# Kernel optimization log

Hardware: AMD Instinct MI355X
Metric: run time of the kernel (lower is better)

The kernel has to match this reference:

```python
import jax, jax.numpy as jnp
import numpy as np

B, S, E, H = 2, 2048, 1024, 16
D = E // H  # head_dim = 64

def setup_inputs() -> dict:
    key = jax.random.key(0)
    k1, k2, k3 = jax.random.split(key, 3)
    x = jax.random.normal(k1, (B, S, E), dtype=jnp.float32)
    W_attn = jax.random.normal(k2, (E, 3 * E), dtype=jnp.float32) * 0.02
    b_attn = jnp.zeros((3 * E,), dtype=jnp.float32)
    W_proj = jax.random.normal(k3, (E, E), dtype=jnp.float32) * 0.02
    b_proj = jnp.zeros((E,), dtype=jnp.float32)
    return {"x": x, "W_attn": W_attn, "b_attn": b_attn, "W_proj": W_proj, "b_proj": b_proj}

def reference(x, W_attn, b_attn, W_proj, b_proj):
    bsz, seq, emb = x.shape
    # fused QKV projection (Conv1D == linear with [in,out] weight)
    qkv = x @ W_attn + b_attn                       # [B,S,3E]
    q, k, v = jnp.split(qkv, 3, axis=-1)
    def to_heads(t):
        return t.reshape(bsz, seq, H, D).transpose(0, 2, 1, 3)  # [B,H,S,D]
    q, k, v = to_heads(q), to_heads(k), to_heads(v)
    scale = jnp.float32(D) ** -0.5
    scores = jnp.einsum('bhqd,bhkd->bhqk', q, k) * scale        # [B,H,S,S]
    causal = jnp.tril(jnp.ones((seq, seq), dtype=bool))
    scores = jnp.where(causal, scores, jnp.float32(-jnp.inf))
    attn = jax.nn.softmax(scores, axis=-1)
    out = jnp.einsum('bhqk,bhkd->bhqd', attn, v)                # [B,H,S,D]
    out = out.transpose(0, 2, 1, 3).reshape(bsz, seq, emb)
    y = out @ W_proj + b_proj
    return y
```

## Files before the change

kernel.cpp:

```cpp
#include <hip/hip_runtime.h>
#include <hip/hip_bf16.h>


typedef __bf16 bf16;
typedef __bf16 bf16x4 __attribute__((ext_vector_type(4)));
typedef __bf16 bf16x8 __attribute__((ext_vector_type(8)));
typedef float  f32x4  __attribute__((ext_vector_type(4)));

#define MNEG (-1.0e30f)
#define QSCALE 0.1803368801f

__device__ __forceinline__ void gload16(const bf16* g, bf16* l) {
  __builtin_amdgcn_global_load_lds((const __attribute__((address_space(1))) void*)g,
                                   (__attribute__((address_space(3))) void*)l, 16, 0, 0);
}

__global__ __launch_bounds__(256) void prep_k(const float* __restrict__ x, bf16* __restrict__ xb,
                                              const float* __restrict__ Wa, bf16* __restrict__ WaT,
                                              const float* __restrict__ Wp, bf16* __restrict__ WpT) {
  const int bid = blockIdx.x;
  if (bid < 2048) {
    const int i = bid * 256 + threadIdx.x;
    f32x4 a = ((const f32x4*)x)[2 * i], b = ((const f32x4*)x)[2 * i + 1];
    bf16x8 o;
    for (int j = 0; j < 4; ++j) { o[j] = (bf16)a[j]; o[4 + j] = (bf16)b[j]; }
    ((bf16x8*)xb)[i] = o;
    return;
  }
  __shared__ bf16 t[64][68];
  const float* in; bf16* out; int C, cx, cy;
  if (bid < 2816) { in = Wa; out = WaT; C = 3072; const int tt = bid - 2048; cx = tt % 48; cy = tt / 48; }
  else            { in = Wp; out = WpT; C = 1024; const int tt = bid - 2816; cx = tt % 16; cy = tt / 16; }
  const int R = 1024;
  const int c0 = cx * 64, r0 = cy * 64;
  const int lr = threadIdx.x >> 4;
  const int lc = (threadIdx.x & 15) * 4;
  for (int i = 0; i < 4; ++i) {
    int r = lr + i * 16;
    f32x4 v = *(const f32x4*)(in + (size_t)(r0 + r) * C + c0 + lc);
    bf16x4 b;
    for (int j = 0; j < 4; ++j) b[j] = (bf16)v[j];
    *(bf16x4*)&t[r][lc] = b;
  }
  __syncthreads();
  for (int i = 0; i < 4; ++i) {
    int c = lr + i * 16;
    bf16x4 v;
    for (int j = 0; j < 4; ++j) v[j] = t[lc + j][c];
    *(bf16x4*)(out + (size_t)(c0 + c) * R + r0 + lc) = v;
  }
}

__global__ __launch_bounds__(512) void gemm_qkv(const bf16* __restrict__ A,
                                                const bf16* __restrict__ Bt,
                                                const float* __restrict__ bias,
                                                bf16* __restrict__ Qo,
                                                bf16* __restrict__ Ko,
                                                bf16* __restrict__ Vo,
                                                int M, int N, int K) {
  __shared__ bf16 As[2][128 * 32];
  __shared__ bf16 Bs[2][128 * 32];
  const int tid = threadIdx.x;
  const int w = tid >> 6, l = tid & 63;
  const int nx = gridDim.x;
  const int nwg = nx * gridDim.y;
  const int flat = blockIdx.y * nx + blockIdx.x;
  const int swz = (flat & 7) * (nwg >> 3) + (flat >> 3);
  const int m0 = (swz / nx) * 128, n0 = (swz % nx) * 128;
  const int wm = w >> 2, wn = w & 3;
  const int fr = l & 15, fg = l >> 4;
  const int grow = tid >> 2;
  const int gcol = (tid & 3) * 8;

  f32x4 acc[4][2] = {};

  auto stage = [&](int k0, int buf) {
    gload16(A  + (size_t)(m0 + grow) * K + k0 + gcol, As[buf] + 512 * w);
    gload16(Bt + (size_t)(n0 + grow) * K + k0 + gcol, Bs[buf] + 512 * w);
  };

  stage(0, 0);

  int cur = 0;
  for (int k0 = 0; k0 < K; k0 += 32) {
    const bool havenext = (k0 + 32 < K);
    if (havenext) stage(k0 + 32, cur ^ 1);

    if (havenext) asm volatile("s_waitcnt vmcnt(2)" ::: "memory");
    else          asm volatile("s_waitcnt vmcnt(0)" ::: "memory");
    __builtin_amdgcn_s_barrier();
    asm volatile("" ::: "memory");

    const bf16* as = As[cur];
    const bf16* bs = Bs[cur];
    bf16x8 af[4], bfv[2];
    for (int mt = 0; mt < 4; ++mt)
      af[mt] = *(const bf16x8*)(as + (wm * 64 + mt * 16 + fr) * 32 + 8 * fg);
    for (int nt = 0; nt < 2; ++nt)
      bfv[nt] = *(const bf16x8*)(bs + (wn * 32 + nt * 16 + fr) * 32 + 8 * fg);
    for (int mt = 0; mt < 4; ++mt)
      for (int nt = 0; nt < 2; ++nt)
        acc[mt][nt] = __builtin_amdgcn_mfma_f32_16x16x32_bf16(af[mt], bfv[nt], acc[mt][nt], 0, 0, 0);

    asm volatile("s_waitcnt lgkmcnt(0)" ::: "memory");
    __builtin_amdgcn_sched_barrier(0);
    __builtin_amdgcn_s_barrier();
    cur ^= 1;
  }

  for (int mt = 0; mt < 4; ++mt) {
    for (int nt = 0; nt < 2; ++nt) {
      const int row0 = m0 + wm * 64 + mt * 16 + 4 * fg;
      const int col = n0 + wn * 32 + nt * 16 + fr;
      const float bv = bias[col];
      const int which = col >> 10, h = (col >> 6) & 15, d = col & 63;
      const int b = row0 >> 11, s = row0 & 2047;
      if (which == 2) {
        bf16x4 vv;
        for (int r = 0; r < 4; ++r) vv[r] = (bf16)(acc[mt][nt][r] + bv);
        *(bf16x4*)(Vo + ((size_t)(b * 16 + h) * 64 + d) * 2048 + s) = vv;
      } else if (which == 0) {
        for (int r = 0; r < 4; ++r)
          Qo[((size_t)(b * 16 + h) * 2048 + s + r) * 64 + d] =
              (bf16)((acc[mt][nt][r] + bv) * QSCALE);
      } else {
        for (int r = 0; r < 4; ++r)
          Ko[((size_t)(b * 16 + h) * 2048 + s + r) * 64 + d] = (bf16)(acc[mt][nt][r] + bv);
      }
    }
  }
}

__global__ __launch_bounds__(512) void gemm_proj(const bf16* __restrict__ A,
                                                 const bf16* __restrict__ Bt,
                                                 const float* __restrict__ bias,
                                                 float* __restrict__ C,
                                                 int M, int N, int K) {
  constexpr int BN = 64, WN = 2, WM = 4, MR = 32, MT = 2;
  __shared__ bf16 As0[128 * 32], As1[128 * 32];
  __shared__ bf16 Bs0[BN * 32],  Bs1[BN * 32];
  const int tid = threadIdx.x;
  const int w = tid >> 6, l = tid & 63;
  const int nx = gridDim.x;
  const int nwg = nx * gridDim.y;
  const int flat = blockIdx.y * nx + blockIdx.x;
  const int swz = (flat & 7) * (nwg >> 3) + (flat >> 3);
  const int m0 = (swz / nx) * 128, n0 = (swz % nx) * BN;
  const int wm = w / WN, wn = w % WN;
  const int fr = l & 15, fg = l >> 4;
  const int grow = tid >> 2;
  const int gcol = (tid & 3) * 8;

  f32x4 acc[MT][2] = {};

  for (int k0 = 0; k0 < K; k0 += 64) {
    __syncthreads();
    gload16(A + (size_t)(m0 + grow) * K + k0 + gcol,      As0 + 512 * w);
    gload16(A + (size_t)(m0 + grow) * K + k0 + 32 + gcol, As1 + 512 * w);
    if (w < 4) {
      gload16(Bt + (size_t)(n0 + grow) * K + k0 + gcol,      Bs0 + 512 * w);
      gload16(Bt + (size_t)(n0 + grow) * K + k0 + 32 + gcol, Bs1 + 512 * w);
    }
    __syncthreads();

    bf16x8 af[MT][2], bfv[2][2];
    for (int mt = 0; mt < MT; ++mt) {
      af[mt][0] = *(const bf16x8*)(As0 + (wm * MR + mt * 16 + fr) * 32 + 8 * fg);
      af[mt][1] = *(const bf16x8*)(As1 + (wm * MR + mt * 16 + fr) * 32 + 8 * fg);
    }
    for (int nt = 0; nt < 2; ++nt) {
      bfv[nt][0] = *(const bf16x8*)(Bs0 + (wn * 32 + nt * 16 + fr) * 32 + 8 * fg);
      bfv[nt][1] = *(const bf16x8*)(Bs1 + (wn * 32 + nt * 16 + fr) * 32 + 8 * fg);
    }
    for (int mt = 0; mt < MT; ++mt)
      for (int nt = 0; nt < 2; ++nt) {
        acc[mt][nt] = __builtin_amdgcn_mfma_f32_16x16x32_bf16(af[mt][0], bfv[nt][0], acc[mt][nt], 0, 0, 0);
        acc[mt][nt] = __builtin_amdgcn_mfma_f32_16x16x32_bf16(af[mt][1], bfv[nt][1], acc[mt][nt], 0, 0, 0);
      }
  }

  for (int mt = 0; mt < MT; ++mt)
    for (int nt = 0; nt < 2; ++nt) {
      const int row0 = m0 + wm * MR + mt * 16 + 4 * fg;
      const int col = n0 + wn * 32 + nt * 16 + fr;
      const float bv = bias[col];
      for (int r = 0; r < 4; ++r)
        C[(size_t)(row0 + r) * N + col] = acc[mt][nt][r] + bv;
    }
}

__global__ __launch_bounds__(256, 3) void attn_k(const bf16* __restrict__ Qw,
                                                 const bf16* __restrict__ Kw,
                                                 const bf16* __restrict__ VtG,
                                                 bf16* __restrict__ AO) {
  __shared__ bf16 Ks[128 * 72];
  __shared__ bf16 Vt[64 * 136];
  __shared__ bf16 Ps[4 * 16 * 72];
  const int tid = threadIdx.x, w = tid >> 6, l = tid & 63;
  const int bid = blockIdx.x;
  const int bh = ((bid & 7) << 2) | ((bid >> 3) & 3);
  const int qt = 31 - (bid >> 5);
  const int q0 = qt * 64;
  const int fr = l & 15, fg = l >> 4;
  const size_t base = (size_t)bh * 2048 * 64;
  const int qw0 = q0 + w * 16;
  const int q = qw0 + fr;
  bf16* Pw = Ps + w * 16 * 72;
  const int r8 = tid >> 3, c8 = (tid & 7) * 8;
  const int r16 = tid >> 4, c16 = (tid & 15) * 8;

  bf16x8 qf[2];
  for (int t = 0; t < 2; ++t)
    qf[t] = *(const bf16x8*)(Qw + base + (size_t)(qw0 + fr) * 64 + 32 * t + 8 * fg);

  f32x4 oacc[4] = {};
  float lsum = 0.f;
  bf16x8 kreg[4], vreg[4];

  auto load_tile = [&](int kt) {
    for (int c = 0; c < 4; ++c) {
      kreg[c] = *(const bf16x8*)(Kw + base + (size_t)(kt + r8 + 32 * c) * 64 + c8);
      vreg[c] = *(const bf16x8*)(VtG + base + (size_t)(r16 + 16 * c) * 2048 + kt + c16);
    }
  };
  auto write_tile = [&]() {
    for (int c = 0; c < 4; ++c) {
      *(bf16x8*)(Ks + (r8 + 32 * c) * 72 + c8) = kreg[c];
      *(bf16x8*)(Vt + (r16 + 16 * c) * 136 + c16) = vreg[c];
    }
  };

  load_tile(0);
  write_tile();
  __syncthreads();

  for (int kt = 0; kt <= q0; kt += 128) {
    const bool havenext = (kt + 128 <= q0);
    if (havenext) load_tile(kt + 128);

    for (int h = 0; h < 2; ++h) {
      const int kh = kt + 64 * h;
      if (kh > q0) break;

      f32x4 sc[4];
      __builtin_amdgcn_s_setprio(1);
      for (int c = 0; c < 4; ++c) {
        bf16x8 kf0 = *(const bf16x8*)(Ks + (64 * h + c * 16 + fr) * 72 + 8 * fg);
        bf16x8 kf1 = *(const bf16x8*)(Ks + (64 * h + c * 16 + fr) * 72 + 32 + 8 * fg);
        f32x4 z = {};
        z = __builtin_amdgcn_mfma_f32_16x16x32_bf16(kf0, qf[0], z, 0, 0, 0);
        sc[c] = __builtin_amdgcn_mfma_f32_16x16x32_bf16(kf1, qf[1], z, 0, 0, 0);
      }
      __builtin_amdgcn_s_setprio(0);

      const bool need_mask = (kh + 63 > qw0);
      float psum = 0.f;
      for (int c = 0; c < 4; ++c) {
        bf16x4 pb;
        for (int r = 0; r < 4; ++r) {
          float s = sc[c][r];
          if (need_mask && (kh + c * 16 + 4 * fg + r > q)) s = MNEG;
          const float pv = __builtin_amdgcn_exp2f(s);
          psum += pv;
          pb[r] = (bf16)pv;
        }
        *(bf16x4*)(Pw + fr * 72 + c * 16 + 4 * fg) = pb;
      }
      psum += __shfl_xor(psum, 16, 64);
      psum += __shfl_xor(psum, 32, 64);
      lsum += psum;

      asm volatile("" ::: "memory");
      __builtin_amdgcn_s_setprio(1);
      for (int t = 0; t < 2; ++t) {
        bf16x8 pa = *(const bf16x8*)(Pw + fr * 72 + 32 * t + 8 * fg);
        for (int dt = 0; dt < 4; ++dt) {
          bf16x8 vf = *(const bf16x8*)(Vt + (dt * 16 + fr) * 136 + 64 * h + 32 * t + 8 * fg);
          oacc[dt] = __builtin_amdgcn_mfma_f32_16x16x32_bf16(pa, vf, oacc[dt], 0, 0, 0);
        }
      }
      __builtin_amdgcn_s_setprio(0);
      asm volatile("" ::: "memory");
    }

    if (!havenext) break;
    __syncthreads();
    write_tile();
    __syncthreads();
  }

  const int b = bh >> 4, h = bh & 15;
  float linv[4];
  for (int r = 0; r < 4; ++r)
    linv[r] = 1.f / __shfl(lsum, (l & 48) | (4 * fg + r), 64);
  for (int dt = 0; dt < 4; ++dt)
    for (int r = 0; r < 4; ++r) {
      const int qq = qw0 + 4 * fg + r;
      AO[(size_t)(b * 2048 + qq) * 1024 + h * 64 + dt * 16 + fr] =
          (bf16)(oacc[dt][r] * linv[r]);
    }
}

extern "C" void kernel_launch(void* const* d_in, const int* in_sizes, int n_in,
                              void* d_out, int out_size, void* d_ws, size_t ws_size,
                              hipStream_t stream) {
  const float* x      = (const float*)d_in[0];
  const float* W_attn = (const float*)d_in[1];
  const float* b_attn = (const float*)d_in[2];
  const float* W_proj = (const float*)d_in[3];
  const float* b_proj = (const float*)d_in[4];
  float* out = (float*)d_out;

  char* ws = (char*)d_ws;
  bf16* WaT = (bf16*)(ws);
  bf16* WpT = (bf16*)(ws + 6291456);
  bf16* Qw  = (bf16*)(ws + 8388608);
  bf16* Kw  = (bf16*)(ws + 16777216);
  bf16* VtG = (bf16*)(ws + 25165824);
  bf16* AO  = (bf16*)(ws + 33554432);
  bf16* xb  = AO;

  prep_k<<<3072, 256, 0, stream>>>(x, xb, W_attn, WaT, W_proj, WpT);

  gemm_qkv<<<dim3(24, 32), 512, 0, stream>>>(
      xb, WaT, b_attn, Qw, Kw, VtG, 4096, 3072, 1024);

  attn_k<<<1024, 256, 0, stream>>>(Qw, Kw, VtG, AO);

  gemm_proj<<<dim3(16, 32), 512, 0, stream>>>(
      AO, WpT, b_proj, out, 4096, 1024, 1024);
}
```

Before: 106.6 us.

## Double-buffer proj GEMM loads and enlarge attention blocks to 128 queries

The output-projection GEMM now uses a two-stage LDS double buffer with K-steps of 32. It issues the next tile's async global-to-LDS loads before computing on the current one and uses explicit vmcnt waits instead of two full barriers per iteration. The attention kernel moves to 512-thread blocks covering 128 query rows (8 waves), so each K/V tile staged in shared memory is reused by twice as many waves. Per-wave skipping of fully masked key halves is added. This trades fewer, larger blocks (and fewer blocks per CU) for less K/V load traffic, and adds more barriers to the GEMM loop.

```diff
diff --git a/kernel.cpp b/kernel.cpp
--- a/kernel.cpp
+++ b/kernel.cpp
@@ -136,52 +136,64 @@
                                                  const float* __restrict__ bias,
                                                  float* __restrict__ C,
                                                  int M, int N, int K) {
-  constexpr int BN = 64, WN = 2, WM = 4, MR = 32, MT = 2;
-  __shared__ bf16 As0[128 * 32], As1[128 * 32];
-  __shared__ bf16 Bs0[BN * 32],  Bs1[BN * 32];
+  __shared__ bf16 As[2][128 * 32];
+  __shared__ bf16 Bs[2][64 * 32];
   const int tid = threadIdx.x;
   const int w = tid >> 6, l = tid & 63;
   const int nx = gridDim.x;
   const int nwg = nx * gridDim.y;
   const int flat = blockIdx.y * nx + blockIdx.x;
   const int swz = (flat & 7) * (nwg >> 3) + (flat >> 3);
-  const int m0 = (swz / nx) * 128, n0 = (swz % nx) * BN;
-  const int wm = w / WN, wn = w % WN;
+  const int m0 = (swz / nx) * 128, n0 = (swz % nx) * 64;
+  const int wm = w >> 1, wn = w & 1;
   const int fr = l & 15, fg = l >> 4;
   const int grow = tid >> 2;
   const int gcol = (tid & 3) * 8;
 
-  f32x4 acc[MT][2] = {};
-
-  for (int k0 = 0; k0 < K; k0 += 64) {
-    __syncthreads();
-    gload16(A + (size_t)(m0 + grow) * K + k0 + gcol,      As0 + 512 * w);
-    gload16(A + (size_t)(m0 + grow) * K + k0 + 32 + gcol, As1 + 512 * w);
-    if (w < 4) {
-      gload16(Bt + (size_t)(n0 + grow) * K + k0 + gcol,      Bs0 + 512 * w);
-      gload16(Bt + (size_t)(n0 + grow) * K + k0 + 32 + gcol, Bs1 + 512 * w);
-    }
-    __syncthreads();
-
-    bf16x8 af[MT][2], bfv[2][2];
-    for (int mt = 0; mt < MT; ++mt) {
-      af[mt][0] = *(const bf16x8*)(As0 + (wm * MR + mt * 16 + fr) * 32 + 8 * fg);
-      af[mt][1] = *(const bf16x8*)(As1 + (wm * MR + mt * 16 + fr) * 32 + 8 * fg);
-    }
+  f32x4 acc[2][2] = {};
+
+  auto stage = [&](int k0, int buf) {
+    gload16(A + (size_t)(m0 + grow) * K + k0 + gcol, As[buf] + 512 * w);
+    if (w < 4)
+      gload16(Bt + (size_t)(n0 + w * 16 + (l >> 2)) * K + k0 + (l & 3) * 8, Bs[buf] + 512 * w);
+  };
+
+  stage(0, 0);
+
+  int cur = 0;
+  for (int k0 = 0; k0 < K; k0 += 32) {
+    const bool havenext = (k0 + 32 < K);
+    if (havenext) stage(k0 + 32, cur ^ 1);
+
+    if (havenext) {
+      if (w < 4) asm volatile("s_waitcnt vmcnt(2)" ::: "memory");
+      else       asm volatile("s_waitcnt vmcnt(1)" ::: "memory");
+    } else {
+      asm volatile("s_waitcnt vmcnt(0)" ::: "memory");
+    }
+    __builtin_amdgcn_s_barrier();
+    asm volatile("" ::: "memory");
+
+    const bf16* as = As[cur];
+    const bf16* bs = Bs[cur];
+    bf16x8 af[2], bfv[2];
+    for (int mt = 0; mt < 2; ++mt)
+      af[mt] = *(const bf16x8*)(as + (wm * 32 + mt * 16 + fr) * 32 + 8 * fg);
+    for (int nt = 0; nt < 2; ++nt)
+      bfv[nt] = *(const bf16x8*)(bs + (wn * 32 + nt * 16 + fr) * 32 + 8 * fg);
+    for (int mt = 0; mt < 2; ++mt)
+      for (int nt = 0; nt < 2; ++nt)
+        acc[mt][nt] = __builtin_amdgcn_mfma_f32_16x16x32_bf16(af[mt], bfv[nt], acc[mt][nt], 0, 0, 0);
+
+    asm volatile("s_waitcnt lgkmcnt(0)" ::: "memory");
+    __builtin_amdgcn_sched_barrier(0);
+    __builtin_amdgcn_s_barrier();
+    cur ^= 1;
+  }
+
+  for (int mt = 0; mt < 2; ++mt)
     for (int nt = 0; nt < 2; ++nt) {
-      bfv[nt][0] = *(const bf16x8*)(Bs0 + (wn * 32 + nt * 16 + fr) * 32 + 8 * fg);
-      bfv[nt][1] = *(const bf16x8*)(Bs1 + (wn * 32 + nt * 16 + fr) * 32 + 8 * fg);
-    }
-    for (int mt = 0; mt < MT; ++mt)
-      for (int nt = 0; nt < 2; ++nt) {
-        acc[mt][nt] = __builtin_amdgcn_mfma_f32_16x16x32_bf16(af[mt][0], bfv[nt][0], acc[mt][nt], 0, 0, 0);
-        acc[mt][nt] = __builtin_amdgcn_mfma_f32_16x16x32_bf16(af[mt][1], bfv[nt][1], acc[mt][nt], 0, 0, 0);
-      }
-  }
-
-  for (int mt = 0; mt < MT; ++mt)
-    for (int nt = 0; nt < 2; ++nt) {
-      const int row0 = m0 + wm * MR + mt * 16 + 4 * fg;
+      const int row0 = m0 + wm * 32 + mt * 16 + 4 * fg;
       const int col = n0 + wn * 32 + nt * 16 + fr;
       const float bv = bias[col];
       for (int r = 0; r < 4; ++r)
@@ -189,18 +201,18 @@
     }
 }
 
-__global__ __launch_bounds__(256, 3) void attn_k(const bf16* __restrict__ Qw,
+__global__ __launch_bounds__(512, 2) void attn_k(const bf16* __restrict__ Qw,
                                                  const bf16* __restrict__ Kw,
                                                  const bf16* __restrict__ VtG,
                                                  bf16* __restrict__ AO) {
   __shared__ bf16 Ks[128 * 72];
   __shared__ bf16 Vt[64 * 136];
-  __shared__ bf16 Ps[4 * 16 * 72];
+  __shared__ bf16 Ps[8 * 16 * 72];
   const int tid = threadIdx.x, w = tid >> 6, l = tid & 63;
   const int bid = blockIdx.x;
   const int bh = ((bid & 7) << 2) | ((bid >> 3) & 3);
-  const int qt = 31 - (bid >> 5);
-  const int q0 = qt * 64;
+  const int qt = 15 - (bid >> 5);
+  const int q0 = qt * 128;
   const int fr = l & 15, fg = l >> 4;
   const size_t base = (size_t)bh * 2048 * 64;
   const int qw0 = q0 + w * 16;
@@ -215,18 +227,18 @@
 
   f32x4 oacc[4] = {};
   float lsum = 0.f;
-  bf16x8 kreg[4], vreg[4];
+  bf16x8 kreg[2], vreg[2];
 
   auto load_tile = [&](int kt) {
-    for (int c = 0; c < 4; ++c) {
-      kreg[c] = *(const bf16x8*)(Kw + base + (size_t)(kt + r8 + 32 * c) * 64 + c8);
-      vreg[c] = *(const bf16x8*)(VtG + base + (size_t)(r16 + 16 * c) * 2048 + kt + c16);
+    for (int c = 0; c < 2; ++c) {
+      kreg[c] = *(const bf16x8*)(Kw + base + (size_t)(kt + r8 + 64 * c) * 64 + c8);
+      vreg[c] = *(const bf16x8*)(VtG + base + (size_t)(r16 + 32 * c) * 2048 + kt + c16);
     }
   };
   auto write_tile = [&]() {
-    for (int c = 0; c < 4; ++c) {
-      *(bf16x8*)(Ks + (r8 + 32 * c) * 72 + c8) = kreg[c];
-      *(bf16x8*)(Vt + (r16 + 16 * c) * 136 + c16) = vreg[c];
+    for (int c = 0; c < 2; ++c) {
+      *(bf16x8*)(Ks + (r8 + 64 * c) * 72 + c8) = kreg[c];
+      *(bf16x8*)(Vt + (r16 + 32 * c) * 136 + c16) = vreg[c];
     }
   };
 
@@ -234,13 +246,15 @@
   write_tile();
   __syncthreads();
 
-  for (int kt = 0; kt <= q0; kt += 128) {
-    const bool havenext = (kt + 128 <= q0);
+  const int ktlim = q0 + 64;
+  for (int kt = 0; kt <= ktlim; kt += 128) {
+    const bool havenext = (kt + 128 <= ktlim);
     if (havenext) load_tile(kt + 128);
 
     for (int h = 0; h < 2; ++h) {
       const int kh = kt + 64 * h;
-      if (kh > q0) break;
+      if (kh > ktlim) break;
+      if (kh > qw0 + 15) continue;
 
       f32x4 sc[4];
       __builtin_amdgcn_s_setprio(1);
@@ -325,7 +339,7 @@
   gemm_qkv<<<dim3(24, 32), 512, 0, stream>>>(
       xb, WaT, b_attn, Qw, Kw, VtG, 4096, 3072, 1024);
 
-  attn_k<<<1024, 256, 0, stream>>>(Qw, Kw, VtG, AO);
+  attn_k<<<512, 512, 0, stream>>>(Qw, Kw, VtG, AO);
 
   gemm_proj<<<dim3(16, 32), 512, 0, stream>>>(
       AO, WpT, b_proj, out, 4096, 1024, 1024);
```

After: 114.8 us. +7.7%, slower.
